# Optimization experiments

Measured on AMD Instinct MI355X. Metric: run time of the kernel, lower is better.

Reference implementation:

```python
import jax, jax.numpy as jnp
import numpy as np
import math

N, T, S, D = 4, 4096, 4096, 256


def setup_inputs() -> dict:
    key = jax.random.key(0)
    ks = jax.random.split(key, 9)
    query = jax.random.normal(ks[0], (N, T, D), dtype=jnp.float32)
    k_in = jax.random.normal(ks[1], (N, S, D), dtype=jnp.float32)
    v_in = jax.random.normal(ks[2], (N, S, D), dtype=jnp.float32)
    # causal boolean mask: True = keep, False = -inf (masked_fill on mask==0)
    attn_mask = jnp.tril(jnp.ones((T, S), dtype=bool))
    s = 1.0 / math.sqrt(D)
    Wq = jax.random.normal(ks[3], (D, D), dtype=jnp.float32) * s
    bq = jax.random.normal(ks[4], (D,), dtype=jnp.float32) * 0.01
    Wk = jax.random.normal(ks[5], (D, D), dtype=jnp.float32) * s
    bk = jax.random.normal(ks[6], (D,), dtype=jnp.float32) * 0.01
    Wv = jax.random.normal(ks[7], (D, D), dtype=jnp.float32) * s
    bv = jax.random.normal(ks[8], (D,), dtype=jnp.float32) * 0.01
    return {"query": query, "key": k_in, "value": v_in, "attn_mask": attn_mask,
            "Wq": Wq, "bq": bq, "Wk": Wk, "bk": bk, "Wv": Wv, "bv": bv}


def reference(query, key, value, attn_mask, Wq, bq, Wk, bk, Wv, bv):
    d = query.shape[-1]
    q = query @ Wq.T + bq            # (N,T,D)
    k = key @ Wk.T + bk              # (N,S,D)
    v = value @ Wv.T + bv            # (N,S,D)
    scores = jnp.einsum('ntd,nsd->nts', q, k)  # (N,T,S) full attention matrix
    additive = jnp.where(attn_mask, jnp.float32(0.0), -jnp.inf)  # (T,S), broadcasts over N
    scores = (scores + additive) / jnp.sqrt(jnp.float32(d))
    attn = jax.nn.softmax(scores, axis=-1)
    # dropout p=0.0 (eval semantics) -> identity
    y = jnp.einsum('nts,nsd->ntd', attn, v)
    return y
```

## Files before the change

kernel.cpp:

```cpp
#include <hip/hip_runtime.h>
#include <hip/hip_bf16.h>

typedef __bf16 bf16;
typedef __attribute__((ext_vector_type(8))) __bf16 bf16x8;
typedef __attribute__((ext_vector_type(4))) __bf16 bf16x4;
typedef __attribute__((ext_vector_type(4))) float f32x4;


static __device__ __forceinline__ unsigned swz(unsigned off, unsigned row) {
  return off ^ ((row & 7u) << 4);
}

__global__ void detect_dtype_kernel(const unsigned* __restrict__ q, int* __restrict__ flag) {
  int t = threadIdx.x;
  int cnt = 0;
  for (int i = t; i < 256; i += 64) {
    unsigned ex = (q[i] >> 7) & 0xFFu;
    cnt += (ex >= 100u && ex <= 140u) ? 1 : 0;
  }
  #pragma unroll
  for (int off = 32; off; off >>= 1) cnt += __shfl_down(cnt, off);
  if (t == 0) *flag = (cnt >= 200) ? 1 : 0;
}

__global__ __launch_bounds__(256) void proj_kernel(
    const void* __restrict__ xq, const void* __restrict__ xk, const void* __restrict__ xv,
    const void* __restrict__ Wq, const void* __restrict__ bq,
    const void* __restrict__ Wk, const void* __restrict__ bk,
    const void* __restrict__ Wv, const void* __restrict__ bv,
    bf16* __restrict__ Qo, bf16* __restrict__ Ko, bf16* __restrict__ Vt,
    const int* __restrict__ flagp)
{
  const int proj = blockIdx.z;
  const void* X  = proj == 0 ? xq : (proj == 1 ? xk : xv);
  const void* W  = proj == 0 ? Wq : (proj == 1 ? Wk : Wv);
  const void* Bp = proj == 0 ? bq : (proj == 1 ? bk : bv);
  const int i0 = blockIdx.x * 64;
  const int j0 = blockIdx.y * 128;
  const int isbf = *flagp;

  __shared__ __align__(16) char lds[24576];
  char* A_lds = lds;
  char* W_lds = lds + 8192;
  const int t = threadIdx.x;

  f32x4 af32[4], wf32[8];
  bf16x8 ab16[2], wb16[4];

  auto load_chunk = [&](int kc) {
    if (isbf) {
      #pragma unroll
      for (int i = 0; i < 2; ++i) {
        int cidx = t + i * 256;
        int row = cidx >> 3, c8 = cidx & 7;
        ab16[i] = *(const bf16x8*)((const char*)X + ((size_t)(i0 + row) << 9) + (kc << 7) + (c8 << 4));
      }
      #pragma unroll
      for (int i = 0; i < 4; ++i) {
        int cidx = t + i * 256;
        int row = cidx >> 3, c8 = cidx & 7;
        wb16[i] = *(const bf16x8*)((const char*)W + ((size_t)(j0 + row) << 9) + (kc << 7) + (c8 << 4));
      }
    } else {
      #pragma unroll
      for (int i = 0; i < 4; ++i) {
        int cidx = t + i * 256;
        int row = cidx >> 4, c4 = cidx & 15;
        af32[i] = *(const f32x4*)((const char*)X + ((size_t)(i0 + row) << 10) + (kc << 8) + (c4 << 4));
      }
      #pragma unroll
      for (int i = 0; i < 8; ++i) {
        int cidx = t + i * 256;
        int row = cidx >> 4, c4 = cidx & 15;
        wf32[i] = *(const f32x4*)((const char*)W + ((size_t)(j0 + row) << 10) + (kc << 8) + (c4 << 4));
      }
    }
  };
  auto write_chunk = [&]() {
    if (isbf) {
      #pragma unroll
      for (int i = 0; i < 2; ++i) {
        int cidx = t + i * 256;
        int row = cidx >> 3, c8 = cidx & 7;
        *(bf16x8*)(A_lds + swz((unsigned)((row << 7) + (c8 << 4)), (unsigned)row)) = ab16[i];
      }
      #pragma unroll
      for (int i = 0; i < 4; ++i) {
        int cidx = t + i * 256;
        int row = cidx >> 3, c8 = cidx & 7;
        *(bf16x8*)(W_lds + swz((unsigned)((row << 7) + (c8 << 4)), (unsigned)row)) = wb16[i];
      }
    } else {
      #pragma unroll
      for (int i = 0; i < 4; ++i) {
        int cidx = t + i * 256;
        int row = cidx >> 4, c4 = cidx & 15;
        bf16x4 ha = { (bf16)af32[i][0], (bf16)af32[i][1], (bf16)af32[i][2], (bf16)af32[i][3] };
        *(bf16x4*)(A_lds + swz((unsigned)((row << 7) + (c4 << 3)), (unsigned)row)) = ha;
      }
      #pragma unroll
      for (int i = 0; i < 8; ++i) {
        int cidx = t + i * 256;
        int row = cidx >> 4, c4 = cidx & 15;
        bf16x4 hw = { (bf16)wf32[i][0], (bf16)wf32[i][1], (bf16)wf32[i][2], (bf16)wf32[i][3] };
        *(bf16x4*)(W_lds + swz((unsigned)((row << 7) + (c4 << 3)), (unsigned)row)) = hw;
      }
    }
  };

  const int w = t >> 6, l = t & 63, lr = l & 15, lhi = l >> 4;
  const int arow = w * 16 + lr;
  f32x4 acc[8] = {};

  load_chunk(0);
  for (int kc = 0; kc < 4; ++kc) {
    write_chunk();
    if (kc < 3) load_chunk(kc + 1);
    __syncthreads();
    #pragma unroll
    for (int kk = 0; kk < 2; ++kk) {
      bf16x8 af = *(const bf16x8*)(A_lds + swz((unsigned)((arow << 7) + (kk << 6) + (lhi << 4)), (unsigned)arow));
      #pragma unroll
      for (int cb = 0; cb < 8; ++cb) {
        int brow = cb * 16 + lr;
        bf16x8 wf = *(const bf16x8*)(W_lds + swz((unsigned)((brow << 7) + (kk << 6) + (lhi << 4)), (unsigned)brow));
        acc[cb] = __builtin_amdgcn_mfma_f32_16x16x32_bf16(af, wf, acc[cb], 0, 0, 0);
      }
    }
    __syncthreads();
  }

  const float QSCALE = 0.09016844005555646f;
  for (int cb = 0; cb < 8; ++cb) {
    int j = j0 + cb * 16 + lr;
    float bias = isbf ? (float)((const bf16*)Bp)[j] : ((const float*)Bp)[j];
    for (int r = 0; r < 4; ++r) {
      int i = i0 + w * 16 + lhi * 4 + r;
      float val = acc[cb][r] + bias;
      if (proj == 0) {
        Qo[((size_t)i << 8) + j] = (bf16)(val * QSCALE);
      } else if (proj == 1) {
        Ko[((size_t)i << 8) + j] = (bf16)val;
      } else {
        int n = i >> 12, s = i & 4095;
        Vt[((size_t)n << 20) + ((size_t)j << 12) + s] = (bf16)val;
      }
    }
  }
}

__global__ __launch_bounds__(256) void attn_kernel(
    const bf16* __restrict__ Q, const bf16* __restrict__ K,
    const bf16* __restrict__ Vt, bf16* __restrict__ Opart, float* __restrict__ wrow)
{
  __shared__ __align__(16) char lds[36864];
  char* K_lds  = lds;
  char* V_lds  = lds + 16384;
  char* P_base = lds + 32768;

  const int n  = blockIdx.y;
  const int bx  = blockIdx.x;
  const int xcd = bx & 7, idx = bx >> 3;
  const int e   = (xcd < 4 ? xcd * 26 : 104 + (xcd - 4) * 25) + idx;
  int g = 0;
  #pragma unroll
  for (int gg = 1; gg <= 5; ++gg) if (e >= 6 * gg * (gg + 1)) g = gg;
  const int r_   = e - 6 * g * (g + 1);
  const int nc   = g + 1;
  const int qoff = r_ / nc;
  const int qi   = 12 * g + qoff;
  const int c    = r_ - qoff * nc;
  const int q0   = qi * 64;
  const int t32  = (qi + 1) * 2;
  const int it0  = c * t32 / nc, it1 = (c + 1) * t32 / nc;

  const int t = threadIdx.x, w = t >> 6, l = t & 63, lr = l & 15, lhi = l >> 4;
  const bf16* Qb = Q  + ((size_t)n << 20);
  const bf16* Kb = K  + ((size_t)n << 20);
  const bf16* Vb = Vt + ((size_t)n << 20);
  char* myP = P_base + (w << 10);

  unsigned gofK[4], lofK[4], gofV[4], lofV[4];
  #pragma unroll
  for (int i = 0; i < 4; ++i) {
    int cidx = t + i * 256;
    int row = cidx >> 5, koff = (cidx & 31) << 4;
    gofK[i] = (unsigned)((row << 9) + koff);
    lofK[i] = swz((unsigned)((row << 9) + koff), (unsigned)row);
    int d = cidx >> 2, soff = (cidx & 3) << 4;
    gofV[i] = (unsigned)((d << 13) + soff);
    lofV[i] = swz((unsigned)((d << 6) + soff), (unsigned)d);
  }
  bf16x8 kst[4], vst[4];
  auto stage_load = [&](int s0) {
    #pragma unroll
    for (int i = 0; i < 4; ++i)
      kst[i] = *(const bf16x8*)((const char*)Kb + (unsigned)(s0 << 9) + gofK[i]);
    #pragma unroll
    for (int i = 0; i < 4; ++i)
      vst[i] = *(const bf16x8*)((const char*)Vb + (unsigned)(s0 << 1) + gofV[i]);
  };

  bf16x8 qf[8];
  {
    int qrow = q0 + w * 16 + lr;
    #pragma unroll
    for (int kb = 0; kb < 8; ++kb)
      qf[kb] = *(const bf16x8*)((const char*)Qb + ((size_t)qrow << 9) + (kb << 6) + (lhi << 4));
  }
  f32x4 o[16] = {};
  float m[4]    = { -3e38f, -3e38f, -3e38f, -3e38f };
  float lsum[4] = { 0.f, 0.f, 0.f, 0.f };

  stage_load(it0 << 5);
  for (int it = it0; it < it1; ++it) {
    #pragma unroll
    for (int i = 0; i < 4; ++i) *(bf16x8*)(K_lds + lofK[i]) = kst[i];
    #pragma unroll
    for (int i = 0; i < 4; ++i) *(bf16x8*)(V_lds + lofV[i]) = vst[i];
    if (it + 1 < it1) stage_load((it + 1) << 5);
    __syncthreads();

    const int s0 = it << 5;
    f32x4 sacc[2];
    #pragma unroll
    for (int cb = 0; cb < 2; ++cb) {
      f32x4 a = {};
      #pragma unroll
      for (int kb = 0; kb < 8; ++kb) {
        int srow = cb * 16 + lr;
        bf16x8 kf = *(const bf16x8*)(K_lds + swz((unsigned)((srow << 9) + (kb << 6) + (lhi << 4)), (unsigned)srow));
        a = __builtin_amdgcn_mfma_f32_16x16x32_bf16(qf[kb], kf, a, 0, 0, 0);
      }
      sacc[cb] = a;
    }

    if (s0 + 31 > q0 + w * 16) {
      #pragma unroll
      for (int cb = 0; cb < 2; ++cb)
        for (int r = 0; r < 4; ++r) {
          int s_ = s0 + cb * 16 + lr;
          int q_ = q0 + w * 16 + lhi * 4 + r;
          if (s_ > q_) sacc[cb][r] = -3e38f;
        }
    }

    float pm[4];
    #pragma unroll
    for (int r = 0; r < 4; ++r) pm[r] = fmaxf(sacc[0][r], sacc[1][r]);
    #pragma unroll
    for (int off = 1; off < 16; off <<= 1)
      for (int r = 0; r < 4; ++r) pm[r] = fmaxf(pm[r], __shfl_xor(pm[r], off));

    unsigned long long need = __ballot((pm[0] > m[0] + 8.f) | (pm[1] > m[1] + 8.f) |
                                       (pm[2] > m[2] + 8.f) | (pm[3] > m[3] + 8.f));
    if (need) {
      float alpha[4];
      #pragma unroll
      for (int r = 0; r < 4; ++r) {
        float mn = fmaxf(m[r], pm[r]);
        alpha[r] = exp2f(m[r] - mn);
        m[r] = mn;
        lsum[r] *= alpha[r];
      }
      #pragma unroll
      for (int db = 0; db < 16; ++db)
        for (int r = 0; r < 4; ++r) o[db][r] *= alpha[r];
    }

    float ps[4] = {};
    #pragma unroll
    for (int cb = 0; cb < 2; ++cb)
      for (int r = 0; r < 4; ++r) {
        float p = exp2f(sacc[cb][r] - m[r]);
        sacc[cb][r] = p;
        ps[r] += p;
      }
    #pragma unroll
    for (int off = 1; off < 16; off <<= 1)
      for (int r = 0; r < 4; ++r) ps[r] += __shfl_xor(ps[r], off);
    #pragma unroll
    for (int r = 0; r < 4; ++r) lsum[r] += ps[r];

    #pragma unroll
    for (int cb = 0; cb < 2; ++cb)
      for (int r = 0; r < 4; ++r) {
        int prow = lhi * 4 + r, pcol = cb * 16 + lr;
        *(bf16*)(myP + swz((unsigned)((prow << 6) + (pcol << 1)), (unsigned)prow)) = (bf16)sacc[cb][r];
      }
    asm volatile("s_waitcnt lgkmcnt(0)" ::: "memory");
    __builtin_amdgcn_sched_barrier(0);

    bf16x8 pf = *(const bf16x8*)(myP + swz((unsigned)((lr << 6) + (lhi << 4)), (unsigned)lr));
    #pragma unroll
    for (int db = 0; db < 16; ++db) {
      int drow = db * 16 + lr;
      bf16x8 vf = *(const bf16x8*)(V_lds + swz((unsigned)((drow << 6) + (lhi << 4)), (unsigned)drow));
      o[db] = __builtin_amdgcn_mfma_f32_16x16x32_bf16(pf, vf, o[db], 0, 0, 0);
    }
    __syncthreads();
  }

  float invl[4];
  #pragma unroll
  for (int r = 0; r < 4; ++r) invl[r] = 1.f / lsum[r];
  bf16* Ob = Opart + (size_t)(n * 204 + e) * 16384;
  for (int db = 0; db < 16; ++db) {
    int col = db * 16 + lr;
    for (int r = 0; r < 4; ++r) {
      int row = w * 16 + lhi * 4 + r;
      Ob[row * 256 + col] = (bf16)(o[db][r] * invl[r]);
    }
  }
  if (lr == 0) {
    #pragma unroll
    for (int r = 0; r < 4; ++r) {
      int row = w * 16 + lhi * 4 + r;
      wrow[(n * 204 + e) * 64 + row] = m[r] + log2f(lsum[r]);
    }
  }
}

__global__ __launch_bounds__(256) void combine_kernel(
    const bf16* __restrict__ Opart, const float* __restrict__ wrow,
    float* __restrict__ out)
{
  const int bx = blockIdx.x, n = blockIdx.y;
  const int qi = bx >> 2, rowbase = (bx & 3) << 4;
  const int g  = qi / 12;
  const int nc = g + 1;
  const int off = 6 * g * (g + 1) + (qi - 12 * g) * nc;
  const int t = threadIdx.x;
  const int row  = rowbase + (t >> 4);
  const int col0 = (t & 15) << 4;
  const size_t pbase = (size_t)(n * 204 + off);

  float u[6];
  float Wm = -3e38f;
  #pragma unroll
  for (int i = 0; i < 6; ++i) {
    u[i] = (i < nc) ? wrow[(pbase + i) * 64 + row] : -3e38f;
    Wm = fmaxf(Wm, u[i]);
  }
  float denom = 0.f;
  #pragma unroll
  for (int i = 0; i < 6; ++i) { u[i] = (i < nc) ? exp2f(u[i] - Wm) : 0.f; denom += u[i]; }
  float inv = 1.f / denom;

  float a[16] = {};
  #pragma unroll
  for (int i = 0; i < 6; ++i) {
    if (i < nc) {
      float ui = u[i] * inv;
      const bf16* p = Opart + (pbase + i) * 16384 + row * 256 + col0;
      bf16x8 v0 = *(const bf16x8*)(p);
      bf16x8 v1 = *(const bf16x8*)(p + 8);
      #pragma unroll
      for (int j = 0; j < 8; ++j) { a[j] += ui * (float)v0[j]; a[8 + j] += ui * (float)v1[j]; }
    }
  }
  float* op = out + ((size_t)n << 20) + ((size_t)(qi * 64 + row) << 8) + col0;
  #pragma unroll
  for (int j2 = 0; j2 < 4; ++j2) {
    f32x4 vv = { a[j2 * 4], a[j2 * 4 + 1], a[j2 * 4 + 2], a[j2 * 4 + 3] };
    *(f32x4*)(op + j2 * 4) = vv;
  }
}

extern "C" void kernel_launch(void* const* d_in, const int* in_sizes, int n_in,
                              void* d_out, int out_size, void* d_ws, size_t ws_size,
                              hipStream_t stream) {
  const void* q_in = d_in[0];
  const void* k_in = d_in[1];
  const void* v_in = d_in[2];
  const void* Wq = d_in[4]; const void* bq = d_in[5];
  const void* Wk = d_in[6]; const void* bk = d_in[7];
  const void* Wv = d_in[8]; const void* bv = d_in[9];

  char* ws = (char*)d_ws;
  bf16*  Qw    = (bf16*)(ws);
  bf16*  Kw    = (bf16*)(ws + (size_t)(8  << 20));
  bf16*  Vtw   = (bf16*)(ws + (size_t)(16 << 20));
  int*   flag  = (int*) (ws + (size_t)(24 << 20));
  float* wrow  = (float*)(ws + (size_t)(24 << 20) + 4096);
  bf16*  Opart = (bf16*)(ws + (size_t)(25 << 20));

  detect_dtype_kernel<<<1, 64, 0, stream>>>((const unsigned*)q_in, flag);
  proj_kernel<<<dim3(256, 2, 3), 256, 0, stream>>>(q_in, k_in, v_in,
                                                   Wq, bq, Wk, bk, Wv, bv,
                                                   Qw, Kw, Vtw, flag);
  attn_kernel<<<dim3(204, 4), 256, 0, stream>>>(Qw, Kw, Vtw, Opart, wrow);
  combine_kernel<<<dim3(256, 4), 256, 0, stream>>>(Opart, wrow, (float*)d_out);
}
```

Measured before the change: 347.1 us.

## Load K and V fragments directly from global memory, dropping LDS staging

Removes the shared-memory staging of K and V tiles along with the register prefetch and the block-wide barriers. Each wave now reads its MFMA operand fragments straight from global memory, and LDS shrinks to the per-wave P buffer. This cuts LDS traffic and __syncthreads stalls and may raise occupancy. In exchange, the four waves each re-read the same K/V data through the cache, and the loads are no longer prefetched ahead, so global latency is exposed.

```diff
diff --git a/kernel.cpp b/kernel.cpp
--- a/kernel.cpp
+++ b/kernel.cpp
@@ -153,11 +153,7 @@
     const bf16* __restrict__ Q, const bf16* __restrict__ K,
     const bf16* __restrict__ Vt, bf16* __restrict__ Opart, float* __restrict__ wrow)
 {
-  __shared__ __align__(16) char lds[36864];
-  char* K_lds  = lds;
-  char* V_lds  = lds + 16384;
-  char* P_base = lds + 32768;
-
+  __shared__ __align__(16) char lds[4096];
   const int n  = blockIdx.y;
   const int bx  = blockIdx.x;
   const int xcd = bx & 7, idx = bx >> 3;
@@ -178,28 +174,7 @@
   const bf16* Qb = Q  + ((size_t)n << 20);
   const bf16* Kb = K  + ((size_t)n << 20);
   const bf16* Vb = Vt + ((size_t)n << 20);
-  char* myP = P_base + (w << 10);
-
-  unsigned gofK[4], lofK[4], gofV[4], lofV[4];
-  #pragma unroll
-  for (int i = 0; i < 4; ++i) {
-    int cidx = t + i * 256;
-    int row = cidx >> 5, koff = (cidx & 31) << 4;
-    gofK[i] = (unsigned)((row << 9) + koff);
-    lofK[i] = swz((unsigned)((row << 9) + koff), (unsigned)row);
-    int d = cidx >> 2, soff = (cidx & 3) << 4;
-    gofV[i] = (unsigned)((d << 13) + soff);
-    lofV[i] = swz((unsigned)((d << 6) + soff), (unsigned)d);
-  }
-  bf16x8 kst[4], vst[4];
-  auto stage_load = [&](int s0) {
-    #pragma unroll
-    for (int i = 0; i < 4; ++i)
-      kst[i] = *(const bf16x8*)((const char*)Kb + (unsigned)(s0 << 9) + gofK[i]);
-    #pragma unroll
-    for (int i = 0; i < 4; ++i)
-      vst[i] = *(const bf16x8*)((const char*)Vb + (unsigned)(s0 << 1) + gofV[i]);
-  };
+  char* myP = lds + (w << 10);
 
   bf16x8 qf[8];
   {
@@ -212,24 +187,17 @@
   float m[4]    = { -3e38f, -3e38f, -3e38f, -3e38f };
   float lsum[4] = { 0.f, 0.f, 0.f, 0.f };
 
-  stage_load(it0 << 5);
   for (int it = it0; it < it1; ++it) {
-    #pragma unroll
-    for (int i = 0; i < 4; ++i) *(bf16x8*)(K_lds + lofK[i]) = kst[i];
-    #pragma unroll
-    for (int i = 0; i < 4; ++i) *(bf16x8*)(V_lds + lofV[i]) = vst[i];
-    if (it + 1 < it1) stage_load((it + 1) << 5);
-    __syncthreads();
-
     const int s0 = it << 5;
+
     f32x4 sacc[2];
     #pragma unroll
     for (int cb = 0; cb < 2; ++cb) {
       f32x4 a = {};
       #pragma unroll
       for (int kb = 0; kb < 8; ++kb) {
-        int srow = cb * 16 + lr;
-        bf16x8 kf = *(const bf16x8*)(K_lds + swz((unsigned)((srow << 9) + (kb << 6) + (lhi << 4)), (unsigned)srow));
+        int srow = s0 + cb * 16 + lr;
+        bf16x8 kf = *(const bf16x8*)((const char*)Kb + ((size_t)srow << 9) + (kb << 6) + (lhi << 4));
         a = __builtin_amdgcn_mfma_f32_16x16x32_bf16(qf[kb], kf, a, 0, 0, 0);
       }
       sacc[cb] = a;
@@ -295,10 +263,11 @@
     #pragma unroll
     for (int db = 0; db < 16; ++db) {
       int drow = db * 16 + lr;
-      bf16x8 vf = *(const bf16x8*)(V_lds + swz((unsigned)((drow << 6) + (lhi << 4)), (unsigned)drow));
+      bf16x8 vf = *(const bf16x8*)((const char*)Vb + ((size_t)drow << 13) + (s0 << 1) + (lhi << 4));
       o[db] = __builtin_amdgcn_mfma_f32_16x16x32_bf16(pf, vf, o[db], 0, 0, 0);
     }
-    __syncthreads();
+    asm volatile("s_waitcnt lgkmcnt(0)" ::: "memory");
+    __builtin_amdgcn_sched_barrier(0);
   }
 
   float invl[4];
```

Result: slower. 504.3 us (+45.3%).
